# Kernel optimization log

Measured on AMD Instinct MI355X. Metric: run time of the kernel, lower is better.

The kernel has to match this reference:

```python
import jax, jax.numpy as jnp
import numpy as np
import math

H = 16        # num heads
D = 64        # head dim
HID = 1024    # hidden size
MULT = 2      # GIN MLP multiplier
FRAC = 0.1    # top_k fraction of available predecessors
THR = 0.2     # threshold value
BASE = 10000.0  # rope base
CHUNK = 32    # query-row chunk for max aggregator
NEG = -1e30


def _rope(x, pos):
    # x: (b, H, S, D); pos: (b, S) int
    d = x.shape[-1]
    inv = 1.0 / (BASE ** (jnp.arange(0, d, 2, dtype=jnp.float32) / d))
    ang = pos.astype(jnp.float32)[..., None] * inv            # (b, S, d//2)
    cos = jnp.concatenate([jnp.cos(ang)] * 2, -1)[:, None]    # (b, 1, S, d)
    sin = jnp.concatenate([jnp.sin(ang)] * 2, -1)[:, None]
    x1, x2 = jnp.split(x, 2, axis=-1)
    return x * cos + jnp.concatenate([-x2, x1], -1) * sin


def _scaled_topk_causal(adj):
    # faithful vectorization of scaled_topk_causal_4d: per query row i, keep
    # top max(1, ceil(FRAC*i)) of the (threshold-filtered) strict predecessors.
    S = adj.shape[-1]
    j = jnp.arange(S)
    strict = j[None, :] < j[:, None]                           # (S, S) j < i
    # torch: filtered = a[:, :i] * (a >= thr)  -> below-threshold become 0
    filtered = jnp.where(strict, jnp.where(adj >= THR, adj, 0.0), NEG)
    order = jnp.argsort(-filtered, axis=-1)                    # descending, stable
    rank = jnp.argsort(order, axis=-1)                         # inverse permutation
    k = jnp.maximum(1, jnp.ceil(FRAC * jnp.arange(S, dtype=jnp.float32))).astype(jnp.int32)
    k = k.at[0].set(0)                                         # row 0 has no predecessors
    return ((rank < k[None, None, :, None]) & strict).astype(adj.dtype)


def reference(hidden_states, Wq, Wk, Wv, Wo, W1, W2, eps, position_ids):
    b, S, _ = hidden_states.shape
    q = (hidden_states @ Wq).reshape(b, S, H, D).transpose(0, 2, 1, 3)
    kk = (hidden_states @ Wk).reshape(b, S, H, D).transpose(0, 2, 1, 3)
    v = (hidden_states @ Wv).reshape(b, S, H, D).transpose(0, 2, 1, 3)
    q = _rope(q, position_ids)
    kk = _rope(kk, position_ids)
    scores = jnp.einsum('bhid,bhjd->bhij', q, kk) / math.sqrt(D)
    adj = _scaled_topk_causal(scores)                          # binary (b,H,S,S)
    deg = adj.sum(-1)                                          # (b,H,S)
    denom = jnp.maximum(deg, 1.0)[..., None]
    s_agg = jnp.einsum('bhij,bhjd->bhid', adj, v)              # sum
    m_agg = s_agg / denom                                      # mean
    var = jnp.maximum(jnp.einsum('bhij,bhjd->bhid', adj, v * v) / denom - m_agg ** 2, 0.0)
    # max aggregator: masked max over selected predecessors, chunked over rows
    nc = S // CHUNK
    adj_c = jnp.moveaxis(adj.reshape(b, H, nc, CHUNK, S), 2, 0)  # (nc,b,H,C,S)
    mx = jax.lax.map(
        lambda ac: jnp.max(jnp.where(ac[..., None] > 0, v[:, :, None, :, :], NEG), axis=-2),
        adj_c)                                                 # (nc,b,H,C,D)
    mx = jnp.moveaxis(mx, 0, 2).reshape(b, H, S, D)
    mx = jnp.where(deg[..., None] > 0, mx, 0.0)
    comb = jnp.concatenate([s_agg, m_agg, mx, var], -1)        # (b,H,S,4D)
    h1 = jax.nn.silu(jnp.einsum('bhsf,hfm->bhsm', comb, W1))   # per-head GIN MLP
    head_out = jnp.einsum('bhsm,hmd->bhsd', h1, W2) + eps * v  # epsilon-scaled residual
    return head_out.transpose(0, 2, 1, 3).reshape(b, S, H * D) @ Wo


def setup_inputs() -> dict:
    key = jax.random.key(0)
    ks = jax.random.split(key, 8)
    b, S = 1, 1024
    sc = 0.02
    return {
        'hidden_states': jax.random.normal(ks[0], (b, S, HID), jnp.float32),
        'Wq': jax.random.normal(ks[1], (HID, H * D), jnp.float32) * sc,
        'Wk': jax.random.normal(ks[2], (HID, H * D), jnp.float32) * sc,
        'Wv': jax.random.normal(ks[3], (HID, H * D), jnp.float32) * sc,
        'Wo': jax.random.normal(ks[4], (H * D, HID), jnp.float32) * sc,
        'W1': jax.random.normal(ks[5], (H, 4 * D, MULT * D), jnp.float32) * sc,
        'W2': jax.random.normal(ks[6], (H, MULT * D, D), jnp.float32) * sc,
        'eps': jnp.asarray(0.1, jnp.float32),
        'position_ids': jnp.arange(S, dtype=jnp.int32)[None, :],
    }
```

## Files before the change

kernel.cpp:

```cpp
#include <hip/hip_runtime.h>
#include <math.h>

#define NEGF  -1e30f
#define TAU   1e-6f

static __device__ __forceinline__ int imin(int a, int b) { return a < b ? a : b; }

static __device__ __forceinline__ void fma44(float A[4][4], const float4 xa, const float4 yb) {
  A[0][0] += xa.x * yb.x; A[0][1] += xa.x * yb.y; A[0][2] += xa.x * yb.z; A[0][3] += xa.x * yb.w;
  A[1][0] += xa.y * yb.x; A[1][1] += xa.y * yb.y; A[1][2] += xa.y * yb.z; A[1][3] += xa.y * yb.w;
  A[2][0] += xa.z * yb.x; A[2][1] += xa.z * yb.y; A[2][2] += xa.z * yb.z; A[2][3] += xa.z * yb.w;
  A[3][0] += xa.w * yb.x; A[3][1] += xa.w * yb.y; A[3][2] += xa.w * yb.z; A[3][3] += xa.w * yb.w;
}

static __device__ __forceinline__ void fold44(float T[4][4], float A[4][4]) {
#pragma unroll
  for (int e = 0; e < 4; ++e)
#pragma unroll
    for (int f = 0; f < 4; ++f) { T[e][f] = __fadd_rn(T[e][f], A[e][f]); A[e][f] = 0.0f; }
}

template <int MODE>
__global__ __launch_bounds__(256) void gemm64(
    const float* __restrict__ A, const float* __restrict__ B, float* __restrict__ C,
    const float* __restrict__ R, const float* __restrict__ eps_p,
    int M, int N, int K, int lda, int ldb, int ldc,
    long sA, long sB, long sC)
{
  const int z = blockIdx.z;
  A += (long)z * sA;
  B += (long)z * sB;
  float* Cf = C + (long)z * sC;
  const float* Rz = (MODE == 2) ? (R + (long)z * sC) : nullptr;

  const int bm = blockIdx.x * 64;
  const int bn = blockIdx.y * 64;
  const int tid = threadIdx.x;
  const int r0 = (tid >> 4) * 4;
  const int c0 = (tid & 15) * 4;

  __shared__ float As[16][68];
  __shared__ float Bs[16][64];

  float acc[4][4] = {};

  const int ar = tid >> 2;
  const int ac = (tid & 3) * 4;
  const int br = tid >> 4;
  const int bc = (tid & 15) * 4;

  for (int kt = 0; kt < K; kt += 16) {
    float4 av = *(const float4*)(A + (long)(bm + ar) * lda + kt + ac);
    float4 bv = *(const float4*)(B + (long)(kt + br) * ldb + bn + bc);
    As[ac + 0][ar] = av.x;
    As[ac + 1][ar] = av.y;
    As[ac + 2][ar] = av.z;
    As[ac + 3][ar] = av.w;
    *(float4*)&Bs[br][bc] = bv;
    __syncthreads();
#pragma unroll
    for (int kk = 0; kk < 16; ++kk) {
      const float4 xa = *(const float4*)&As[kk][r0];
      const float4 yb = *(const float4*)&Bs[kk][c0];
      fma44(acc, xa, yb);
    }
    __syncthreads();
  }

  const float ev = (MODE == 2) ? eps_p[0] : 0.0f;
#pragma unroll
  for (int e = 0; e < 4; ++e)
#pragma unroll
    for (int f = 0; f < 4; ++f) {
      const int r = bm + r0 + e;
      const int c = bn + c0 + f;
      float x = acc[e][f];
      if (MODE == 1) x = x / (1.0f + expf(-x));
      if (MODE == 2) x += ev * Rz[(long)r * ldc + c];
      Cf[(long)r * ldc + c] = x;
    }
}

__global__ __launch_bounds__(256) void gemm_qkv64(
    const float* __restrict__ A,
    const float* __restrict__ Wq, const float* __restrict__ Wk, const float* __restrict__ Wv,
    float* __restrict__ qo, float* __restrict__ ko, float* __restrict__ vo)
{
  const int z = blockIdx.z;
  const float* B = (z == 0) ? Wq : (z == 1) ? Wk : Wv;
  float* C = (z == 0) ? qo : (z == 1) ? ko : vo;

  const int bm = blockIdx.x * 64;
  const int bn = blockIdx.y * 64;
  const int tid = threadIdx.x;
  const int r0 = (tid >> 4) * 4;
  const int c0 = (tid & 15) * 4;

  __shared__ float As[2][32][68];
  __shared__ float Bs[2][32][64];

  float acc[4][4] = {};
  float tot[4][4] = {};

  const int ar = tid >> 2;
  const int ac = (tid & 3) * 8;
  const int br = tid >> 3;
  const int bc = (tid & 7) * 8;

  {
    float4 a0 = *(const float4*)(A + (long)(bm + ar) * 1024 + ac);
    float4 a1 = *(const float4*)(A + (long)(bm + ar) * 1024 + ac + 4);
    float4 b0 = *(const float4*)(B + (long)br * 1024 + bn + bc);
    float4 b1 = *(const float4*)(B + (long)br * 1024 + bn + bc + 4);
    As[0][ac + 0][ar] = a0.x; As[0][ac + 1][ar] = a0.y;
    As[0][ac + 2][ar] = a0.z; As[0][ac + 3][ar] = a0.w;
    As[0][ac + 4][ar] = a1.x; As[0][ac + 5][ar] = a1.y;
    As[0][ac + 6][ar] = a1.z; As[0][ac + 7][ar] = a1.w;
    *(float4*)&Bs[0][br][bc] = b0;
    *(float4*)&Bs[0][br][bc + 4] = b1;
  }
  __syncthreads();

  int cur = 0;
  for (int kt = 0; kt < 1024; kt += 32) {
    const bool more = (kt + 32 < 1024);
    float4 a0n, a1n, b0n, b1n;
    if (more) {
      a0n = *(const float4*)(A + (long)(bm + ar) * 1024 + kt + 32 + ac);
      a1n = *(const float4*)(A + (long)(bm + ar) * 1024 + kt + 32 + ac + 4);
      b0n = *(const float4*)(B + (long)(kt + 32 + br) * 1024 + bn + bc);
      b1n = *(const float4*)(B + (long)(kt + 32 + br) * 1024 + bn + bc + 4);
    }
    if (kt == 384 || kt == 768) {
      fold44(tot, acc);
    }
#pragma unroll
    for (int kk = 0; kk < 32; ++kk) {
      const float4 xa = *(const float4*)&As[cur][kk][r0];
      const float4 yb = *(const float4*)&Bs[cur][kk][c0];
      fma44(acc, xa, yb);
    }
    if (more) {
      const int nxt = cur ^ 1;
      As[nxt][ac + 0][ar] = a0n.x; As[nxt][ac + 1][ar] = a0n.y;
      As[nxt][ac + 2][ar] = a0n.z; As[nxt][ac + 3][ar] = a0n.w;
      As[nxt][ac + 4][ar] = a1n.x; As[nxt][ac + 5][ar] = a1n.y;
      As[nxt][ac + 6][ar] = a1n.z; As[nxt][ac + 7][ar] = a1n.w;
      *(float4*)&Bs[nxt][br][bc] = b0n;
      *(float4*)&Bs[nxt][br][bc + 4] = b1n;
      __syncthreads();
      cur = nxt;
    }
  }

#pragma unroll
  for (int e = 0; e < 4; ++e)
#pragma unroll
    for (int f = 0; f < 4; ++f)
      C[(long)(bm + r0 + e) * 1024 + bn + c0 + f] = __fadd_rn(tot[e][f], acc[e][f]);
}

__global__ __launch_bounds__(256) void combine_out(
    const float4* __restrict__ p, float4* __restrict__ dst)
{
  const int idx = blockIdx.x * 256 + threadIdx.x;
  const float4 a = p[idx];
  const float4 b = p[idx + (1 << 18)];
  float4 r;
  r.x = __fadd_rn(a.x, b.x);
  r.y = __fadd_rn(a.y, b.y);
  r.z = __fadd_rn(a.z, b.z);
  r.w = __fadd_rn(a.w, b.w);
  dst[idx] = r;
}

__global__ __launch_bounds__(256) void rope_table(
    const int* __restrict__ pos_ids, float2* __restrict__ tab)
{
  const int g = blockIdx.x * 256 + threadIdx.x;
  const int t = g & 31;
  const int s = g >> 5;

  const float e = (float)(2 * t) / 64.0f;
  const float p32 = (float)pow(10000.0, (double)e);
  const float inv = __fdiv_rn(1.0f, p32);
  const float posf = (float)pos_ids[s];
  const float ang = __fmul_rn(posf, inv);
  tab[g] = make_float2((float)cos((double)ang), (float)sin((double)ang));
}

__global__ __launch_bounds__(256) void rope_apply(float* __restrict__ q,
                                                  float* __restrict__ kb,
                                                  const float2* __restrict__ tab)
{
  const int g = blockIdx.x * blockDim.x + threadIdx.x;
  const int t = g & 31;
  const int h = (g >> 5) & 15;
  const int s = (g >> 9) & 1023;
  const int buf = g >> 19;
  float* p = buf ? kb : q;

  const float2 cs = tab[s * 32 + t];
  const float c  = cs.x;
  const float sn = cs.y;

  const int base = s * 1024 + h * 64;
  const float x1 = p[base + t];
  const float x2 = p[base + t + 32];
  p[base + t]      = __fadd_rn(__fmul_rn(x1, c), __fmul_rn(-x2, sn));
  p[base + t + 32] = __fadd_rn(__fmul_rn(x2, c), __fmul_rn(x1, sn));
}

__global__ __launch_bounds__(256) void gemm_score(
    const float* __restrict__ q, const float* __restrict__ kb,
    float* __restrict__ S, int headBase)
{
  const int x = blockIdx.x;
  int bmT = 0;
  while ((bmT + 1) * (bmT + 2) / 2 <= x) ++bmT;
  const int bnT = x - bmT * (bmT + 1) / 2;

  const int hl = blockIdx.y;
  const int off = (headBase + hl) * 64;
  const int bm = bmT * 64;
  const int bn = bnT * 64;
  const int tid = threadIdx.x;
  const int r0 = (tid >> 4) * 4;
  const int c0 = (tid & 15) * 4;

  __shared__ float As[16][68];
  __shared__ float Bs[16][68];

  float acc[4][4] = {};

  const int ar = tid >> 2;
  const int ac = (tid & 3) * 4;

  for (int kt = 0; kt < 64; kt += 16) {
    float4 av = *(const float4*)(q  + (long)(bm + ar) * 1024 + off + kt + ac);
    float4 bv = *(const float4*)(kb + (long)(bn + ar) * 1024 + off + kt + ac);
    As[ac + 0][ar] = av.x; As[ac + 1][ar] = av.y;
    As[ac + 2][ar] = av.z; As[ac + 3][ar] = av.w;
    Bs[ac + 0][ar] = bv.x; Bs[ac + 1][ar] = bv.y;
    Bs[ac + 2][ar] = bv.z; Bs[ac + 3][ar] = bv.w;
    __syncthreads();
#pragma unroll
    for (int kk = 0; kk < 16; ++kk) {
      const float4 xa = *(const float4*)&As[kk][r0];
      const float4 yb = *(const float4*)&Bs[kk][c0];
      fma44(acc, xa, yb);
    }
    __syncthreads();
  }

#pragma unroll
  for (int e = 0; e < 4; ++e)
#pragma unroll
    for (int f = 0; f < 4; ++f)
      S[((long)hl * 1024 + bm + r0 + e) * 1024 + bn + c0 + f] = acc[e][f] * 0.125f;
}

__global__ __launch_bounds__(256) void select_agg3(
    const float* __restrict__ S, const float* __restrict__ v,
    float* __restrict__ comb, int headBase)
{
  const int tid = threadIdx.x;
  const int lane = tid & 63;
  const int wid = tid >> 6;
  const int i = blockIdx.x * 4 + wid;
  const int hl = blockIdx.y;
  const int h = headBase + hl;

  __shared__ int histS[4][256];
  __shared__ unsigned listS[4][128];
  int* hist = histS[wid];
  unsigned* list = listS[wid];

  const int jb = lane * 16;
  const int njc = i - jb;
  const int nj = njc < 0 ? 0 : (njc > 16 ? 16 : njc);

  const float* row = S + ((long)hl * 1024 + i) * 1024;
  float raw[16];
  unsigned uf[16];
  {
    const float4 r0 = *(const float4*)(row + jb);
    const float4 r1 = *(const float4*)(row + jb + 4);
    const float4 r2 = *(const float4*)(row + jb + 8);
    const float4 r3 = *(const float4*)(row + jb + 12);
    raw[0]=r0.x; raw[1]=r0.y; raw[2]=r0.z; raw[3]=r0.w;
    raw[4]=r1.x; raw[5]=r1.y; raw[6]=r1.z; raw[7]=r1.w;
    raw[8]=r2.x; raw[9]=r2.y; raw[10]=r2.z; raw[11]=r2.w;
    raw[12]=r3.x; raw[13]=r3.y; raw[14]=r3.z; raw[15]=r3.w;
  }
#pragma unroll
  for (int m = 0; m < 16; ++m) {
    const float rv = (m < nj) ? raw[m] : 0.0f;
    raw[m] = rv;
    uf[m] = (m < nj && rv >= 0.2f) ? __float_as_uint(rv) : 0u;
  }

  const int kk = (i > 0) ? (i + 9) / 10 : 0;
  unsigned V = 0u;
  int need_eq = 0;
  unsigned fmask = 0u;

  if (kk > 0) {
    unsigned prefix = 0;
    int rk = kk;
    bool done = false;
    for (int pass = 0; pass < 4 && !done; ++pass) {
      const int shift = 24 - 8 * pass;
      *(int4*)&hist[lane * 4] = make_int4(0, 0, 0, 0);
      asm volatile("s_waitcnt lgkmcnt(0)" ::: "memory");
      __builtin_amdgcn_sched_barrier(0);
#pragma unroll
      for (int m = 0; m < 16; ++m) {
        const unsigned u = uf[m];
        if (m < nj && u != 0u && (pass == 0 || (u >> (shift + 8)) == prefix))
          atomicAdd(&hist[(u >> shift) & 0xFF], 1);
      }
      asm volatile("s_waitcnt lgkmcnt(0)" ::: "memory");
      __builtin_amdgcn_sched_barrier(0);
      const int4 hv = *(const int4*)&hist[lane * 4];
      const int s = hv.x + hv.y + hv.z + hv.w;
      int suf = s;
#pragma unroll
      for (int off = 1; off < 64; off <<= 1) {
        const int o = __shfl_down(suf, off, 64);
        if (lane + off < 64) suf += o;
      }
      const int tot = __shfl(suf, 0, 64);
      if (pass == 0 && tot < rk) {
        V = 0u; need_eq = rk - tot; done = true;
      } else {
        const int above = suf - s;
        const int sfx3 = above + hv.w;
        const int sfx2 = sfx3 + hv.z;
        const int sfx1 = sfx2 + hv.y;
        const int sfx0 = suf;
        int mbin = -1, mh = 0, msfx = 0;
        if (!(pass == 0 && lane == 0) && sfx0 >= rk && sfx0 - hv.x < rk) { mbin = lane * 4 + 0; mh = hv.x; msfx = sfx0; }
        if (sfx1 >= rk && sfx1 - hv.y < rk) { mbin = lane * 4 + 1; mh = hv.y; msfx = sfx1; }
        if (sfx2 >= rk && sfx2 - hv.z < rk) { mbin = lane * 4 + 2; mh = hv.z; msfx = sfx2; }
        if (sfx3 >= rk && sfx3 - hv.w < rk) { mbin = lane * 4 + 3; mh = hv.w; msfx = sfx3; }
        const unsigned long long bal = __ballot(mbin >= 0);
        const int src = (int)__ffsll((unsigned long long)bal) - 1;
        const int selBin = __shfl(mbin, src, 64) & 0xFF;
        const int scnt = __shfl(mh, src, 64);
        const int ssfx = __shfl(msfx, src, 64);
        prefix = (prefix << 8) | (unsigned)selBin;
        rk = rk - (ssfx - scnt);
        if (rk == scnt) {
          unsigned vm = 0xFFFFFFFFu;
#pragma unroll
          for (int m = 0; m < 16; ++m) {
            const unsigned u = uf[m];
            if (m < nj && u != 0u && (u >> shift) == prefix && u < vm) vm = u;
          }
#pragma unroll
          for (int off = 1; off < 64; off <<= 1) {
            const unsigned o = (unsigned)__shfl_xor((int)vm, off, 64);
            if (o < vm) vm = o;
          }
          V = vm; need_eq = 0x3FFFFFFF; done = true;
        }
      }
    }
    if (!done) { V = prefix; need_eq = rk; }

    int e = 0;
#pragma unroll
    for (int m = 0; m < 16; ++m) if (m < nj && uf[m] == V) ++e;
    int val = e;
#pragma unroll
    for (int off = 1; off < 64; off <<= 1) {
      const int n = __shfl_up(val, off, 64);
      if (lane >= off) val += n;
    }
    int excl = val - e;
#pragma unroll
    for (int m = 0; m < 16; ++m) if (m < nj) {
      const unsigned u = uf[m];
      if (u > V) fmask |= (1u << m);
      else if (u == V) { if (excl < need_eq) fmask |= (1u << m); ++excl; }
    }
  }

  int hypOut = -1, hypIn = -1;
  if (kk > 0 && kk < i) {
    unsigned wmax = 0u;
    int mIn = -1;
    unsigned long long tbIn = ~0ull, tbOut = ~0ull;
#pragma unroll
    for (int m = 0; m < 16; ++m) if (m < nj) {
      const int j = jb + m;
      const unsigned u = uf[m];
      if ((fmask >> m) & 1u) {
        if (u == V && j > mIn) mIn = j;
        const float fv = __uint_as_float(u);
        const float dd = fv - 0.2f;
        if (fv >= 0.2f && dd < TAU) {
          const unsigned long long p = (((unsigned long long)__float_as_uint(dd)) << 32) | (unsigned)j;
          if (p < tbIn) tbIn = p;
        }
      } else {
        if (u > wmax) wmax = u;
        if (raw[m] < 0.2f) {
          const float dd = 0.2f - raw[m];
          if (dd < TAU) {
            const unsigned long long p = (((unsigned long long)__float_as_uint(dd)) << 32) | (unsigned)j;
            if (p < tbOut) tbOut = p;
          }
        }
      }
    }
#pragma unroll
    for (int off = 1; off < 64; off <<= 1) {
      const unsigned ow = (unsigned)__shfl_xor((int)wmax, off, 64);
      if (ow > wmax) wmax = ow;
      const int om = __shfl_xor(mIn, off, 64);
      if (om > mIn) mIn = om;
      const unsigned long long oi = __shfl_xor(tbIn, off, 64);
      if (oi < tbIn) tbIn = oi;
      const unsigned long long oo = __shfl_xor(tbOut, off, 64);
      if (oo < tbOut) tbOut = oo;
    }
    int outMin = 0x7FFFFFFF;
#pragma unroll
    for (int m = 0; m < 16; ++m) if (m < nj) {
      if (!((fmask >> m) & 1u) && uf[m] == wmax) {
        const int j = jb + m;
        if (j < outMin) outMin = j;
      }
    }
#pragma unroll
    for (int off = 1; off < 64; off <<= 1) {
      const int o = __shfl_xor(outMin, off, 64);
      if (o < outMin) outMin = o;
    }
    float bestD = TAU;
    int oI = -1, nI = -1;
    if (outMin != 0x7FFFFFFF && mIn >= 0) {
      const float Vf = __uint_as_float(V);
      const float Wf = __uint_as_float(wmax);
      if (!(wmax == V && V == 0u)) {
        const float gapA = Vf - Wf;
        if (gapA < bestD) { bestD = gapA; oI = mIn; nI = outMin; }
      }
      if (tbIn != ~0ull) {
        const float d = __uint_as_float((unsigned)(tbIn >> 32));
        const int jj = (int)(tbIn & 0xFFFFFFFFu);
        const bool noop = (wmax == 0u && jj < outMin);
        if (!noop && d < bestD) { bestD = d; oI = jj; nI = outMin; }
      }
      if (tbOut != ~0ull && Vf <= 0.2f) {
        const float d = __uint_as_float((unsigned)(tbOut >> 32));
        const int jj = (int)(tbOut & 0xFFFFFFFFu);
        if (d < bestD) { bestD = d; oI = mIn; nI = jj; }
      }
    }
    hypOut = oI; hypIn = nI;
  }

  const bool amb = (hypOut >= 0);
  unsigned smask = 0u;
  int cnt = 0;
#pragma unroll
  for (int m = 0; m < 16; ++m) if (m < nj) {
    const int j = jb + m;
    int s1 = (int)((fmask >> m) & 1u);
    if (amb) { if (j == hypOut) s1 = 0; if (j == hypIn) s1 = 1; }
    if (s1) smask |= (1u << m);
    if (((fmask >> m) & 1u) | (unsigned)s1) ++cnt;
  }
  int val2 = cnt;
#pragma unroll
  for (int off = 1; off < 64; off <<= 1) {
    const int n = __shfl_up(val2, off, 64);
    if (lane >= off) val2 += n;
  }
  const int L = __shfl(val2, 63, 64);
  int base = val2 - cnt;
#pragma unroll
  for (int m = 0; m < 16; ++m) if (m < nj) {
    const unsigned f0b = (fmask >> m) & 1u;
    const unsigned s1b = (smask >> m) & 1u;
    if (f0b | s1b) {
      list[base] = (unsigned)(jb + m) | (f0b << 10) | (s1b << 11);
      ++base;
    }
  }
  asm volatile("s_waitcnt lgkmcnt(0)" ::: "memory");
  __builtin_amdgcn_sched_barrier(0);

  float sum0 = 0, sq0 = 0, mx0 = NEGF, sum1 = 0, sq1 = 0, mx1 = NEGF;
  const float* vcol = v + h * 64 + lane;
  for (int e2 = 0; e2 < L; e2 += 4) {
    const uint4 en4 = *(const uint4*)&list[e2];
    const unsigned w0 = (e2 + 0 < L) ? en4.x : 0u;
    const unsigned w1 = (e2 + 1 < L) ? en4.y : 0u;
    const unsigned w2 = (e2 + 2 < L) ? en4.z : 0u;
    const unsigned w3 = (e2 + 3 < L) ? en4.w : 0u;
    float v0 = 0, v1 = 0, v2 = 0, v3 = 0;
    if (w0) v0 = vcol[(long)(w0 & 1023) * 1024];
    if (w1) v1 = vcol[(long)(w1 & 1023) * 1024];
    if (w2) v2 = vcol[(long)(w2 & 1023) * 1024];
    if (w3) v3 = vcol[(long)(w3 & 1023) * 1024];
    if (w0 & (1u << 10)) { sum0 += v0; sq0 += v0 * v0; mx0 = fmaxf(mx0, v0); }
    if (w0 & (1u << 11)) { sum1 += v0; sq1 += v0 * v0; mx1 = fmaxf(mx1, v0); }
    if (w1 & (1u << 10)) { sum0 += v1; sq0 += v1 * v1; mx0 = fmaxf(mx0, v1); }
    if (w1 & (1u << 11)) { sum1 += v1; sq1 += v1 * v1; mx1 = fmaxf(mx1, v1); }
    if (w2 & (1u << 10)) { sum0 += v2; sq0 += v2 * v2; mx0 = fmaxf(mx0, v2); }
    if (w2 & (1u << 11)) { sum1 += v2; sq1 += v2 * v2; mx1 = fmaxf(mx1, v2); }
    if (w3 & (1u << 10)) { sum0 += v3; sq0 += v3 * v3; mx0 = fmaxf(mx0, v3); }
    if (w3 & (1u << 11)) { sum1 += v3; sq1 += v3 * v3; mx1 = fmaxf(mx1, v3); }
  }

  const float denom = (float)(kk > 0 ? kk : 1);
  const float mean0 = sum0 / denom, mean1 = sum1 / denom;
  const float var0 = fmaxf(sq0 / denom - mean0 * mean0, 0.0f);
  const float var1 = fmaxf(sq1 / denom - mean1 * mean1, 0.0f);
  const float mx0o = (kk > 0) ? mx0 : 0.0f;
  const float mx1o = (kk > 0) ? mx1 : 0.0f;
  float* crow = comb + ((long)(h * 1024 + i)) * 256;
  crow[lane]       = 0.5f * (sum0 + sum1);
  crow[64 + lane]  = 0.5f * (mean0 + mean1);
  crow[128 + lane] = 0.5f * (mx0o + mx1o);
  crow[192 + lane] = 0.5f * (var0 + var1);
}

extern "C" void kernel_launch(void* const* d_in, const int* in_sizes, int n_in,
                              void* d_out, int out_size, void* d_ws, size_t ws_size,
                              hipStream_t stream)
{
  const float* hidden = (const float*)d_in[0];
  const float* Wq = (const float*)d_in[1];
  const float* Wk = (const float*)d_in[2];
  const float* Wv = (const float*)d_in[3];
  const float* Wo = (const float*)d_in[4];
  const float* W1 = (const float*)d_in[5];
  const float* W2 = (const float*)d_in[6];
  const float* eps = (const float*)d_in[7];
  const int* pos = (const int*)d_in[8];

  const size_t MB = 1024UL * 1024UL;
  int G = 4;
  if (ws_size >= 28 * MB + 64 * MB) G = 16;
  else if (ws_size >= 28 * MB + 32 * MB) G = 8;

  float* q      = (float*)d_ws;
  float* kbuf   = q + (1 << 20);
  float* v      = kbuf + (1 << 20);
  float* comb   = v + (1 << 20);
  float* scores = comb + (1 << 22);
  float* h1     = scores;
  float* ho     = scores + (1 << 21);
  float2* tab   = (float2*)comb;
  float* parts  = comb;

  const dim3 blk(256);

  gemm_qkv64<<<dim3(16, 16, 3), blk, 0, stream>>>(hidden, Wq, Wk, Wv, q, kbuf, v);

  rope_table<<<128, blk, 0, stream>>>(pos, tab);
  rope_apply<<<4096, blk, 0, stream>>>(q, kbuf, tab);

  for (int g = 0; g < 16; g += G) {
    gemm_score<<<dim3(136, G), blk, 0, stream>>>(q, kbuf, scores, g);
    select_agg3<<<dim3(256, G), blk, 0, stream>>>(scores, v, comb, g);
  }

  gemm64<1><<<dim3(16, 2, 16), blk, 0, stream>>>(comb, W1, h1, nullptr, nullptr,
      1024, 128, 256, 256, 128, 128, (long)1024 * 256, (long)256 * 128, (long)1024 * 128);

  gemm64<2><<<dim3(16, 1, 16), blk, 0, stream>>>(h1, W2, ho, v, eps,
      1024, 64, 128, 128, 64, 1024, (long)1024 * 128, (long)128 * 64, 64);

  gemm64<0><<<dim3(16, 16, 2), blk, 0, stream>>>(ho, Wo, parts, nullptr, nullptr,
      1024, 1024, 512, 1024, 1024, 1024, 512, (long)512 * 1024, (long)1 << 20);
  combine_out<<<dim3(1024), blk, 0, stream>>>((const float4*)parts, (float4*)d_out);
}
```

Before: 377.9 us.

## Split QKV projection over K into three panels with partial-sum combine

Replaces the single QKV GEMM with a split-K variant that uses 64x128 tiles and divides K into three panels, writing partial results into scratch space, then sums them with a separate combine kernel. The goal is more blocks and more per-thread work for better utilisation of the GPU. In exchange it adds extra global-memory traffic for the partial buffers and one more kernel launch, and the fixed summation order changes rounding. The new path is taken only when the workspace is at least 64 MB.

```diff
diff --git a/kernel.cpp b/kernel.cpp
--- a/kernel.cpp
+++ b/kernel.cpp
@@ -79,6 +79,104 @@
       if (MODE == 2) x += ev * Rz[(long)r * ldc + c];
       Cf[(long)r * ldc + c] = x;
     }
+}
+
+__global__ __launch_bounds__(256) void gemm_qkv_s48(
+    const float* __restrict__ A,
+    const float* __restrict__ Wq, const float* __restrict__ Wk, const float* __restrict__ Wv,
+    float* __restrict__ part)
+{
+  const int z = blockIdx.z;
+  const int mat = z % 3;
+  const int panel = z / 3;
+  const float* B = (mat == 0) ? Wq : (mat == 1) ? Wk : Wv;
+  float* P = part + ((long)(mat * 3 + panel) << 20);
+
+  const int k0 = panel * 384;
+  const int k1 = (panel == 2) ? 1024 : (k0 + 384);
+
+  const int bm = blockIdx.x * 64;
+  const int bn = blockIdx.y * 128;
+  const int tid = threadIdx.x;
+  const int r0 = (tid >> 4) * 4;
+  const int c0 = (tid & 15) * 8;
+
+  __shared__ float As[2][16][68];
+  __shared__ float Bs[2][16][132];
+
+  float aL[4][4] = {}, aR[4][4] = {};
+
+  const int ar = tid >> 2;
+  const int ac = (tid & 3) * 4;
+  const int br = tid >> 4;
+  const int bc = (tid & 15) * 8;
+
+  {
+    float4 av = *(const float4*)(A + (long)(bm + ar) * 1024 + k0 + ac);
+    float4 b0 = *(const float4*)(B + (long)(k0 + br) * 1024 + bn + bc);
+    float4 b1 = *(const float4*)(B + (long)(k0 + br) * 1024 + bn + bc + 4);
+    As[0][ac + 0][ar] = av.x; As[0][ac + 1][ar] = av.y;
+    As[0][ac + 2][ar] = av.z; As[0][ac + 3][ar] = av.w;
+    *(float4*)&Bs[0][br][bc] = b0;
+    *(float4*)&Bs[0][br][bc + 4] = b1;
+  }
+  __syncthreads();
+
+  int cur = 0;
+  for (int kt = k0; kt < k1; kt += 16) {
+    const bool more = (kt + 16 < k1);
+    float4 avn, b0n, b1n;
+    if (more) {
+      avn = *(const float4*)(A + (long)(bm + ar) * 1024 + kt + 16 + ac);
+      b0n = *(const float4*)(B + (long)(kt + 16 + br) * 1024 + bn + bc);
+      b1n = *(const float4*)(B + (long)(kt + 16 + br) * 1024 + bn + bc + 4);
+    }
+#pragma unroll
+    for (int kk = 0; kk < 16; ++kk) {
+      const float4 xa = *(const float4*)&As[cur][kk][r0];
+      const float4 y0 = *(const float4*)&Bs[cur][kk][c0];
+      const float4 y1 = *(const float4*)&Bs[cur][kk][c0 + 4];
+      fma44(aL, xa, y0);
+      fma44(aR, xa, y1);
+    }
+    if (more) {
+      const int nxt = cur ^ 1;
+      As[nxt][ac + 0][ar] = avn.x; As[nxt][ac + 1][ar] = avn.y;
+      As[nxt][ac + 2][ar] = avn.z; As[nxt][ac + 3][ar] = avn.w;
+      *(float4*)&Bs[nxt][br][bc] = b0n;
+      *(float4*)&Bs[nxt][br][bc + 4] = b1n;
+      __syncthreads();
+      cur = nxt;
+    }
+  }
+
+#pragma unroll
+  for (int e = 0; e < 4; ++e) {
+    float* prow = P + (long)(bm + r0 + e) * 1024 + bn;
+#pragma unroll
+    for (int f = 0; f < 4; ++f) {
+      prow[c0 + f]     = aL[e][f];
+      prow[c0 + 4 + f] = aR[e][f];
+    }
+  }
+}
+
+__global__ __launch_bounds__(256) void combine_qkv(
+    const float4* __restrict__ part, float4* __restrict__ dst)
+{
+  const int idx = blockIdx.x * 256 + threadIdx.x;
+  const int mat = idx >> 18;
+  const int w = idx & 0x3FFFF;
+  const long b = (long)(mat * 3) << 18;
+  const float4 s0 = part[b + w];
+  const float4 s1 = part[b + (1L << 18) + w];
+  const float4 s2 = part[b + (2L << 18) + w];
+  float4 r;
+  r.x = __fadd_rn(__fadd_rn(s0.x, s1.x), s2.x);
+  r.y = __fadd_rn(__fadd_rn(s0.y, s1.y), s2.y);
+  r.z = __fadd_rn(__fadd_rn(s0.z, s1.z), s2.z);
+  r.w = __fadd_rn(__fadd_rn(s0.w, s1.w), s2.w);
+  dst[idx] = r;
 }
 
 __global__ __launch_bounds__(256) void gemm_qkv64(
@@ -561,7 +659,13 @@
 
   const dim3 blk(256);
 
-  gemm_qkv64<<<dim3(16, 16, 3), blk, 0, stream>>>(hidden, Wq, Wk, Wv, q, kbuf, v);
+  if (ws_size >= 64 * MB) {
+    float* part = scores;
+    gemm_qkv_s48<<<dim3(16, 8, 9), blk, 0, stream>>>(hidden, Wq, Wk, Wv, part);
+    combine_qkv<<<dim3(3072), blk, 0, stream>>>((const float4*)part, (float4*)q);
+  } else {
+    gemm_qkv64<<<dim3(16, 16, 3), blk, 0, stream>>>(hidden, Wq, Wk, Wv, q, kbuf, v);
+  }
 
   rope_table<<<128, blk, 0, stream>>>(pos, tab);
   rope_apply<<<4096, blk, 0, stream>>>(q, kbuf, tab);
```

Result: faster. 357.7 us (-5.4%).
